# Kernel optimization log

Measured on AMD Instinct MI355X. Metric: run time of the kernel, lower is better.

## Reference

```python
import jax, jax.numpy as jnp
import numpy as np

L, B, T, D, H, A, F, V, BIAS_DIM, E = 6, 16, 512, 512, 8, 64, 2048, 10000, 4, 200000
LN_EPS = 1e-3  # keras LayerNormalization default


def positional_encoding(d, max_len):
    pos = np.arange(max_len, dtype=np.float32)[:, None]
    i = np.arange(d, dtype=np.float32)[None, :]
    angle = pos / np.power(10000.0, (2.0 * np.floor(i / 2.0)) / d)
    pe = np.where((np.arange(d) % 2) == 0, np.sin(angle), np.cos(angle))
    return jnp.asarray(pe, jnp.float32)


def layer_norm(x, g, b):
    mu = jnp.mean(x, -1, keepdims=True)
    var = jnp.mean(jnp.square(x - mu), -1, keepdims=True)
    return (x - mu) * jax.lax.rsqrt(var + LN_EPS) * g + b


def attention(x, masks, bias_idx, Wq, Wk, Wv, Wo, be, bs):
    q = jnp.einsum('btd,dha->btha', x, Wq)
    k = jnp.einsum('btd,dha->btha', x, Wk)
    v = jnp.einsum('btd,dha->btha', x, Wv)
    alpha = jnp.einsum('bkha,bqha->bhqk', k, q)
    # sparse edge bias: scalar per edge = bias_embs[type] @ bias_scalar
    ev = (be[bias_idx[:, 0]] @ bs)[:, 0]                      # [E]
    dense = jnp.zeros((x.shape[0], x.shape[1], x.shape[1]), x.dtype)
    dense = dense.at[bias_idx[:, 1], bias_idx[:, 2], bias_idx[:, 3]].add(ev)  # scatter_nd semantics (add)
    ksum = jnp.sum(k, -1)                                     # [B,T,H]
    alpha = alpha + jnp.einsum('bqk,bkh->bhqk', dense, ksum)
    alpha = alpha * jax.lax.rsqrt(jnp.float32(A))
    alpha = alpha * masks + (1.0 - jnp.ceil(masks)) * jnp.finfo(jnp.float32).min
    alpha = jax.nn.softmax(alpha, -1)
    ctx = jnp.einsum('bhqk,bkha->bqha', alpha, v)
    return jnp.einsum('btha,had->btd', ctx, Wo)


def setup_inputs() -> dict:
    key = jax.random.key(0)
    ks = jax.random.split(key, 24)
    tokens = jax.random.randint(ks[0], (B, T), 0, V, dtype=jnp.int32)
    masks = jnp.ones((B, 1, T, T), jnp.float32)
    ab = jnp.stack([
        jax.random.randint(ks[1], (E,), 0, BIAS_DIM, dtype=jnp.int32),
        jax.random.randint(ks[2], (E,), 0, B, dtype=jnp.int32),
        jax.random.randint(ks[3], (E,), 0, T, dtype=jnp.int32),
        jax.random.randint(ks[4], (E,), 0, T, dtype=jnp.int32)], axis=1)
    s = 0.03
    return {
        'tokens': tokens, 'masks': masks, 'attention_bias': ab,
        'embed': jax.random.normal(ks[5], (V, D)) * (D ** -0.5),
        'Wq': jax.random.normal(ks[6], (L, D, H, A)) * s,
        'Wk': jax.random.normal(ks[7], (L, D, H, A)) * s,
        'Wv': jax.random.normal(ks[8], (L, D, H, A)) * s,
        'Wo': jax.random.normal(ks[9], (L, H, A, D)) * s,
        'be': jax.random.normal(ks[10], (L, BIAS_DIM, A)) * s,
        'bs': jax.random.normal(ks[11], (L, A, 1)) * s,
        'ln_g': jnp.ones((L, 2, D)), 'ln_b': jnp.zeros((L, 2, D)),
        'ff1_w': jax.random.normal(ks[12], (L, D, F)) * s,
        'ff1_b': jnp.zeros((L, F)),
        'ff2_w': jax.random.normal(ks[13], (L, F, D)) * s,
        'ff2_b': jnp.zeros((L, D)),
        'lnout_g': jnp.ones((D,)), 'lnout_b': jnp.zeros((D,)),
    }


def reference(tokens, masks, attention_bias, embed, Wq, Wk, Wv, Wo, be, bs,
              ln_g, ln_b, ff1_w, ff1_b, ff2_w, ff2_b, lnout_g, lnout_b):
    pos_enc = positional_encoding(D, 5000)
    x = embed[tokens] * jnp.sqrt(jnp.float32(D)) + pos_enc[:T]
    for l in range(L):
        h = layer_norm(x, ln_g[l, 0], ln_b[l, 0])
        x = x + attention(h, masks, attention_bias, Wq[l], Wk[l], Wv[l], Wo[l], be[l], bs[l])
        h = layer_norm(x, ln_g[l, 1], ln_b[l, 1])
        x = x + jax.nn.relu(h @ ff1_w[l] + ff1_b[l]) @ ff2_w[l] + ff2_b[l]
    return layer_norm(x, lnout_g, lnout_b)
```

## Files before the change

kernel.cpp:

```cpp
#include <hip/hip_runtime.h>
#include <hip/hip_bf16.h>

#define LNUM 6
#define BB 16
#define TT 512
#define DD 512
#define HH 8
#define AA 64
#define FFD 2048
#define EE 200000
#define BIASDIM 4
#define ATT_NEG (-3.402823466e38f)

typedef __bf16 bf16_t;
typedef __attribute__((ext_vector_type(8))) __bf16 bf16x8;
typedef __attribute__((ext_vector_type(4))) float f32x4;

typedef __attribute__((address_space(3))) void lds_void;
typedef const __attribute__((address_space(1))) void glb_void;

__device__ __forceinline__ void async_load16(const bf16_t* g, bf16_t* l) {
    __builtin_amdgcn_global_load_lds((glb_void*)g, (lds_void*)l, 16, 0, 0);
}

__global__ __launch_bounds__(256) void embed_pe_kernel(
    const int* __restrict__ tokens, const float* __restrict__ embed,
    float* __restrict__ x)
{
    int idx = blockIdx.x * 256 + threadIdx.x;
    int d  = idx & (DD - 1);
    int bt = idx >> 9;
    int t  = bt & (TT - 1);
    int tok = tokens[bt];
    float e = embed[(long long)tok * DD + d] * 22.62741699796952f;
    float p = (float)(2 * (d >> 1)) * (1.0f / (float)DD);
    float denom = exp2f(p * 13.287712379549449f);
    float angle = (float)t / denom;
    float pe = (d & 1) ? cosf(angle) : sinf(angle);
    x[idx] = e + pe;
}

template <typename TO>
__global__ __launch_bounds__(256) void ln_kernel(
    const float* __restrict__ x, TO* __restrict__ y,
    const float* __restrict__ g, const float* __restrict__ b)
{
    long long row = blockIdx.x;
    const float* xr = x + row * DD;
    int tid = threadIdx.x;
    float v0 = xr[tid], v1 = xr[tid + 256];
    float s = v0 + v1, sq = v0 * v0 + v1 * v1;
#pragma unroll
    for (int o = 32; o > 0; o >>= 1) {
        s  += __shfl_down(s, o);
        sq += __shfl_down(sq, o);
    }
    __shared__ float ss[4], sq4[4];
    if ((tid & 63) == 0) { ss[tid >> 6] = s; sq4[tid >> 6] = sq; }
    __syncthreads();
    float st  = ss[0] + ss[1] + ss[2] + ss[3];
    float sqt = sq4[0] + sq4[1] + sq4[2] + sq4[3];
    float mean = st * (1.0f / DD);
    float var  = sqt * (1.0f / DD) - mean * mean;
    float inv  = rsqrtf(var + 1e-3f);
    y[row * DD + tid]       = (TO)((v0 - mean) * inv * g[tid]       + b[tid]);
    y[row * DD + tid + 256] = (TO)((v1 - mean) * inv * g[tid + 256] + b[tid + 256]);
}

template <typename TO, int S>
__global__ __launch_bounds__(256) void reduce_ln_kernel(
    float* __restrict__ x, const float* __restrict__ P,
    TO* __restrict__ y, const float* __restrict__ g, const float* __restrict__ b)
{
    const long long NXc = (long long)BB * TT * DD;
    long long row = blockIdx.x;
    int tid = threadIdx.x;
    long long i0 = row * DD + tid;
    float v0 = x[i0], v1 = x[i0 + 256];
#pragma unroll
    for (int s = 0; s < S; s++) {
        v0 += P[(long long)s * NXc + i0];
        v1 += P[(long long)s * NXc + i0 + 256];
    }
    x[i0] = v0; x[i0 + 256] = v1;
    float s2 = v0 + v1, sq = v0 * v0 + v1 * v1;
#pragma unroll
    for (int o = 32; o > 0; o >>= 1) {
        s2 += __shfl_down(s2, o);
        sq += __shfl_down(sq, o);
    }
    __shared__ float ss[4], sq4[4];
    if ((tid & 63) == 0) { ss[tid >> 6] = s2; sq4[tid >> 6] = sq; }
    __syncthreads();
    float st  = ss[0] + ss[1] + ss[2] + ss[3];
    float sqt = sq4[0] + sq4[1] + sq4[2] + sq4[3];
    float mean = st * (1.0f / DD);
    float var  = sqt * (1.0f / DD) - mean * mean;
    float inv  = rsqrtf(var + 1e-3f);
    y[i0]       = (TO)((v0 - mean) * inv * g[tid]       + b[tid]);
    y[i0 + 256] = (TO)((v1 - mean) * inv * g[tid + 256] + b[tid + 256]);
}

__global__ __launch_bounds__(256) void ksum_kernel(
    const bf16_t* __restrict__ k, float* __restrict__ ks)
{
    int idx = blockIdx.x * 256 + threadIdx.x;
    long long base = (long long)idx * AA;
    float s = 0.f;
#pragma unroll
    for (int a = 0; a < AA; a++) s += (float)k[base + a];
    ks[idx] = s;
}

__global__ __launch_bounds__(256) void bias_scatter_kernel(
    const int* __restrict__ ab, const float* __restrict__ be,
    const float* __restrict__ bs, float* __restrict__ dense)
{
    __shared__ float ev[BIASDIM];
    int tid = threadIdx.x;
    if (tid < BIASDIM) {
        float s = 0.f;
        for (int a = 0; a < AA; a++) s += be[tid * AA + a] * bs[a];
        ev[tid] = s;
    }
    __syncthreads();
    int e = blockIdx.x * 256 + tid;
    if (e < EE) {
        int ty = ab[e * 4 + 0];
        int b  = ab[e * 4 + 1];
        int q  = ab[e * 4 + 2];
        int kk = ab[e * 4 + 3];
        atomicAdd(&dense[((long long)b * TT + q) * TT + kk], ev[ty]);
    }
}

__global__ __launch_bounds__(256) void wconv_kernel(
    const float* __restrict__ in, bf16_t* __restrict__ out, int R, int Cc)
{
    __shared__ bf16_t tile[64][65];
    int c0 = blockIdx.x * 64, r0 = blockIdx.y * 64;
    int tid = threadIdx.x;
#pragma unroll
    for (int i = 0; i < 16; i++) {
        int idx = tid + i * 256; int r = idx >> 6, c = idx & 63;
        tile[c][r] = (bf16_t)in[(long long)(r0 + r) * Cc + c0 + c];
    }
    __syncthreads();
#pragma unroll
    for (int i = 0; i < 16; i++) {
        int idx = tid + i * 256; int rr = idx >> 6, cc = idx & 63;
        out[(long long)(c0 + rr) * R + r0 + cc] = tile[rr][cc];
    }
}

struct Ptr4 { const float* p[4]; };

__global__ __launch_bounds__(256) void wconv4_kernel(Ptr4 srcs, bf16_t* __restrict__ out)
{
    __shared__ bf16_t tile[64][65];
    int z = blockIdx.z;
    const float* in = srcs.p[z];
    bf16_t* o = out + (long long)z * DD * DD;
    int c0 = blockIdx.x * 64, r0 = blockIdx.y * 64;
    int tid = threadIdx.x;
#pragma unroll
    for (int i = 0; i < 16; i++) {
        int idx = tid + i * 256; int r = idx >> 6, c = idx & 63;
        tile[c][r] = (bf16_t)in[(long long)(r0 + r) * DD + c0 + c];
    }
    __syncthreads();
#pragma unroll
    for (int i = 0; i < 16; i++) {
        int idx = tid + i * 256; int rr = idx >> 6, cc = idx & 63;
        o[(long long)(c0 + rr) * DD + r0 + cc] = tile[rr][cc];
    }
}

__global__ __launch_bounds__(256) void vtrans_kernel(
    const bf16_t* __restrict__ v, bf16_t* __restrict__ vT)
{
    __shared__ bf16_t tile[64][65];
    int bh = blockIdx.y; int b = bh >> 3, h = bh & 7;
    int t0 = blockIdx.x * 64;
    int tid = threadIdx.x;
#pragma unroll
    for (int i = 0; i < 16; i++) {
        int idx = tid + i * 256; int r = idx >> 6, c = idx & 63;
        tile[c][r] = v[((long long)(b * TT + t0 + r) * HH + h) * AA + c];
    }
    __syncthreads();
#pragma unroll
    for (int i = 0; i < 16; i++) {
        int idx = tid + i * 256; int a = idx >> 6, t2 = idx & 63;
        vT[(((long long)b * HH + h) * AA + a) * TT + t0 + t2] = tile[a][t2];
    }
}

__global__ __launch_bounds__(256) void fused_attn_kernel(
    const bf16_t* __restrict__ qg, const bf16_t* __restrict__ kg,
    const bf16_t* __restrict__ vT, const float* __restrict__ dense,
    const float* __restrict__ ksum, const float* __restrict__ masks,
    bf16_t* __restrict__ ctx)
{
    __shared__ __align__(16) bf16_t Ks[64 * 64];
    __shared__ __align__(16) bf16_t Vs[64 * 64];
    __shared__ __align__(16) bf16_t Plds[4 * 16 * 88];

    int tid = threadIdx.x;
    int wave = tid >> 6, lane = tid & 63;
    int row16 = lane & 15, quad = lane >> 4;
    int bh = blockIdx.y; int b = bh >> 3, h = bh & 7;
    int qw = blockIdx.x * 64 + wave * 16;

    bf16x8 qf[2];
    {
        const bf16_t* qp = qg + (((long long)b * TT + qw + row16) * HH + h) * AA + quad * 8;
        qf[0] = *(const bf16x8*)(qp);
        qf[1] = *(const bf16x8*)(qp + 32);
    }

    f32x4 o[4] = {};
    float m_r[4], l_r[4];
#pragma unroll
    for (int r = 0; r < 4; r++) { m_r[r] = -3.0e38f; l_r[r] = 0.f; }

    bf16_t* Pw = Plds + wave * 16 * 88;
    const float* dbase = dense + (long long)b * TT * TT;
    const float* mbase = masks + (long long)b * TT * TT;

    for (int kt = 0; kt < 8; kt++) {
        int t0 = kt * 64;
#pragma unroll
        for (int p = tid; p < 512; p += 256) {
            int r = p >> 3, s = p & 7, c = s ^ (r & 7);
            async_load16(kg + (((long long)b * TT + t0 + r) * HH + h) * AA + c * 8,
                         Ks + p * 8);
        }
#pragma unroll
        for (int p = tid; p < 512; p += 256) {
            int r = p >> 3, s = p & 7, c = s ^ (r & 7);
            async_load16(vT + ((long long)bh * AA + r) * TT + t0 + c * 8,
                         Vs + p * 8);
        }
        __syncthreads();

        f32x4 s4[4] = {};
#pragma unroll
        for (int n = 0; n < 4; n++) {
            int row = n * 16 + row16;
            int sw = row & 7;
            bf16x8 kf0 = *(const bf16x8*)(Ks + row * 64 + ((quad ^ sw) * 8));
            bf16x8 kf1 = *(const bf16x8*)(Ks + row * 64 + (((quad + 4) ^ sw) * 8));
            s4[n] = __builtin_amdgcn_mfma_f32_16x16x32_bf16(qf[0], kf0, s4[n], 0, 0, 0);
            s4[n] = __builtin_amdgcn_mfma_f32_16x16x32_bf16(qf[1], kf1, s4[n], 0, 0, 0);
        }

        float val[4][4];
#pragma unroll
        for (int n = 0; n < 4; n++) {
            int ktok = t0 + n * 16 + row16;
            float ksv = ksum[((long long)b * TT + ktok) * HH + h];
#pragma unroll
            for (int r = 0; r < 4; r++) {
                int qgl = qw + quad * 4 + r;
                float d  = dbase[(long long)qgl * TT + ktok];
                float mk = mbase[(long long)qgl * TT + ktok];
                float vv = 0.125f * fmaf(d, ksv, s4[n][r]);
                val[n][r] = vv * mk + (1.0f - ceilf(mk)) * ATT_NEG;
            }
        }

        float scl[4];
#pragma unroll
        for (int r = 0; r < 4; r++) {
            float mx = fmaxf(fmaxf(val[0][r], val[1][r]), fmaxf(val[2][r], val[3][r]));
#pragma unroll
            for (int off = 1; off < 16; off <<= 1) mx = fmaxf(mx, __shfl_xor(mx, off));
            float mnew = fmaxf(m_r[r], mx);
            float sc = __expf(m_r[r] - mnew);
            float ps = 0.f;
#pragma unroll
            for (int n = 0; n < 4; n++) {
                float p = __expf(val[n][r] - mnew);
                val[n][r] = p;
                ps += p;
            }
#pragma unroll
            for (int off = 1; off < 16; off <<= 1) ps += __shfl_xor(ps, off);
            l_r[r] = l_r[r] * sc + ps;
            m_r[r] = mnew;
            scl[r] = sc;
        }
#pragma unroll
        for (int j = 0; j < 4; j++)
#pragma unroll
            for (int r = 0; r < 4; r++) o[j][r] *= scl[r];

#pragma unroll
        for (int n = 0; n < 4; n++)
#pragma unroll
            for (int r = 0; r < 4; r++)
                Pw[(quad * 4 + r) * 88 + n * 16 + row16] = (bf16_t)val[n][r];
        asm volatile("s_waitcnt lgkmcnt(0)" ::: "memory");

        bf16x8 pa0 = *(const bf16x8*)(Pw + row16 * 88 + quad * 8);
        bf16x8 pa1 = *(const bf16x8*)(Pw + row16 * 88 + 32 + quad * 8);
#pragma unroll
        for (int j = 0; j < 4; j++) {
            int row = j * 16 + row16;
            int sw = row & 7;
            bf16x8 vb0 = *(const bf16x8*)(Vs + row * 64 + ((quad ^ sw) * 8));
            bf16x8 vb1 = *(const bf16x8*)(Vs + row * 64 + (((quad + 4) ^ sw) * 8));
            o[j] = __builtin_amdgcn_mfma_f32_16x16x32_bf16(pa0, vb0, o[j], 0, 0, 0);
            o[j] = __builtin_amdgcn_mfma_f32_16x16x32_bf16(pa1, vb1, o[j], 0, 0, 0);
        }
        __syncthreads();
    }

#pragma unroll
    for (int r = 0; r < 4; r++) {
        float invl = 1.0f / l_r[r];
        int qgl = qw + quad * 4 + r;
        bf16_t* cp = ctx + (((long long)b * TT + qgl) * HH + h) * AA;
#pragma unroll
        for (int j = 0; j < 4; j++)
            cp[j * 16 + row16] = (bf16_t)(o[j][r] * invl);
    }
}

template <int BM, int BN, typename TC>
__global__ __launch_bounds__((BM / 64) * (BN / 64) * 64) void gemm_mfma(
    const bf16_t* __restrict__ Ag, const bf16_t* __restrict__ Bg, TC* __restrict__ Cg,
    int K, int lda, int ldb, int ldc,
    long long sAz, long long sBz, long long sCz,
    const float* __restrict__ bias, int accum, int relu)
{
    constexpr int WN = BN / 64;
    constexpr int NT = (BM / 64) * (BN / 64) * 64;
    __shared__ __align__(16) bf16_t As[2][BM * 32];
    __shared__ __align__(16) bf16_t Bs[2][BN * 32];

    int z = blockIdx.z;
    Ag += z * sAz; Bg += z * sBz; Cg += z * sCz;

    int tid = threadIdx.x;
    int wave = tid >> 6, lane = tid & 63;
    int wm = (wave / WN) * 64, wn = (wave % WN) * 64;
    int m0 = blockIdx.x * BM, n0 = blockIdx.y * BN;
    int row16 = lane & 15, quad = lane >> 4;

    f32x4 acc[4][4] = {};

#pragma unroll
    for (int p = tid; p < BM * 4; p += NT) {
        int r = p >> 2, c = p & 3;
        async_load16(Ag + (long long)(m0 + r) * lda + c * 8, As[0] + p * 8);
    }
#pragma unroll
    for (int p = tid; p < BN * 4; p += NT) {
        int r = p >> 2, c = p & 3;
        async_load16(Bg + (long long)(n0 + r) * ldb + c * 8, Bs[0] + p * 8);
    }

    int ib = 0;
    for (int k0 = 0; k0 < K; k0 += 32, ib ^= 1) {
        __syncthreads();
        if (k0 + 32 < K) {
            int kn = k0 + 32;
#pragma unroll
            for (int p = tid; p < BM * 4; p += NT) {
                int r = p >> 2, c = p & 3;
                async_load16(Ag + (long long)(m0 + r) * lda + kn + c * 8,
                             As[ib ^ 1] + p * 8);
            }
#pragma unroll
            for (int p = tid; p < BN * 4; p += NT) {
                int r = p >> 2, c = p & 3;
                async_load16(Bg + (long long)(n0 + r) * ldb + kn + c * 8,
                             Bs[ib ^ 1] + p * 8);
            }
        }
        bf16x8 af[4], bfr[4];
#pragma unroll
        for (int i = 0; i < 4; i++)
            af[i] = *(const bf16x8*)(As[ib] + (wm + i * 16 + row16) * 32 + quad * 8);
#pragma unroll
        for (int j = 0; j < 4; j++)
            bfr[j] = *(const bf16x8*)(Bs[ib] + (wn + j * 16 + row16) * 32 + quad * 8);
#pragma unroll
        for (int i = 0; i < 4; i++)
#pragma unroll
            for (int j = 0; j < 4; j++)
                acc[i][j] = __builtin_amdgcn_mfma_f32_16x16x32_bf16(
                    af[i], bfr[j], acc[i][j], 0, 0, 0);
    }

#pragma unroll
    for (int i = 0; i < 4; i++) {
#pragma unroll
        for (int j = 0; j < 4; j++) {
#pragma unroll
            for (int r = 0; r < 4; r++) {
                int m = m0 + wm + i * 16 + quad * 4 + r;
                int n = n0 + wn + j * 16 + row16;
                float vv = acc[i][j][r];
                if (bias) vv += bias[n];
                if (accum) vv += (float)Cg[(long long)m * ldc + n];
                if (relu) vv = fmaxf(vv, 0.f);
                Cg[(long long)m * ldc + n] = (TC)vv;
            }
        }
    }
}

template <int BM, int BN, int SPLIT>
__global__ __launch_bounds__((BM / 64) * (BN / 64) * 64) void gemm_splitk(
    const bf16_t* __restrict__ Ag, const bf16_t* __restrict__ Bg,
    float* __restrict__ Cg, float* __restrict__ Pg,
    int K, int lda, int ldb, int ldc, const float* __restrict__ bias)
{
    constexpr int WN = BN / 64;
    constexpr int NT = (BM / 64) * (BN / 64) * 64;
    __shared__ __align__(16) bf16_t As[2][BM * 32];
    __shared__ __align__(16) bf16_t Bs[2][BN * 32];

    int z = blockIdx.z;
    int kc = K / SPLIT;
    int kbeg = z * kc, kend = kbeg + kc;

    int tid = threadIdx.x;
    int wave = tid >> 6, lane = tid & 63;
    int wm = (wave / WN) * 64, wn = (wave % WN) * 64;
    int m0 = blockIdx.x * BM, n0 = blockIdx.y * BN;
    int row16 = lane & 15, quad = lane >> 4;

    f32x4 acc[4][4] = {};

#pragma unroll
    for (int p = tid; p < BM * 4; p += NT) {
        int r = p >> 2, c = p & 3;
        async_load16(Ag + (long long)(m0 + r) * lda + kbeg + c * 8, As[0] + p * 8);
    }
#pragma unroll
    for (int p = tid; p < BN * 4; p += NT) {
        int r = p >> 2, c = p & 3;
        async_load16(Bg + (long long)(n0 + r) * ldb + kbeg + c * 8, Bs[0] + p * 8);
    }

    int ib = 0;
    for (int k0 = kbeg; k0 < kend; k0 += 32, ib ^= 1) {
        __syncthreads();
        if (k0 + 32 < kend) {
            int kn = k0 + 32;
#pragma unroll
            for (int p = tid; p < BM * 4; p += NT) {
                int r = p >> 2, c = p & 3;
                async_load16(Ag + (long long)(m0 + r) * lda + kn + c * 8,
                             As[ib ^ 1] + p * 8);
            }
#pragma unroll
            for (int p = tid; p < BN * 4; p += NT) {
                int r = p >> 2, c = p & 3;
                async_load16(Bg + (long long)(n0 + r) * ldb + kn + c * 8,
                             Bs[ib ^ 1] + p * 8);
            }
        }
        bf16x8 af[4], bfr[4];
#pragma unroll
        for (int i = 0; i < 4; i++)
            af[i] = *(const bf16x8*)(As[ib] + (wm + i * 16 + row16) * 32 + quad * 8);
#pragma unroll
        for (int j = 0; j < 4; j++)
            bfr[j] = *(const bf16x8*)(Bs[ib] + (wn + j * 16 + row16) * 32 + quad * 8);
#pragma unroll
        for (int i = 0; i < 4; i++)
#pragma unroll
            for (int j = 0; j < 4; j++)
                acc[i][j] = __builtin_amdgcn_mfma_f32_16x16x32_bf16(
                    af[i], bfr[j], acc[i][j], 0, 0, 0);
    }

    const long long NXc = (long long)BB * TT * DD;
#pragma unroll
    for (int i = 0; i < 4; i++) {
#pragma unroll
        for (int j = 0; j < 4; j++) {
#pragma unroll
            for (int r = 0; r < 4; r++) {
                int m = m0 + wm + i * 16 + quad * 4 + r;
                int n = n0 + wn + j * 16 + row16;
                float vv = acc[i][j][r];
                if (z == 0) {
                    if (bias) vv += bias[n];
                    long long ci = (long long)m * ldc + n;
                    Cg[ci] = Cg[ci] + vv;
                } else {
                    Pg[(long long)(z - 1) * NXc + (long long)m * ldc + n] = vv;
                }
            }
        }
    }
}

extern "C" void kernel_launch(void* const* d_in, const int* in_sizes, int n_in,
                              void* d_out, int out_size, void* d_ws, size_t ws_size,
                              hipStream_t stream)
{
    const int*   tokens = (const int*)d_in[0];
    const float* masks  = (const float*)d_in[1];
    const int*   ab     = (const int*)d_in[2];
    const float* embed  = (const float*)d_in[3];
    const float* Wq     = (const float*)d_in[4];
    const float* Wk     = (const float*)d_in[5];
    const float* Wv     = (const float*)d_in[6];
    const float* Wo     = (const float*)d_in[7];
    const float* be     = (const float*)d_in[8];
    const float* bs     = (const float*)d_in[9];
    const float* ln_g   = (const float*)d_in[10];
    const float* ln_b   = (const float*)d_in[11];
    const float* ff1w   = (const float*)d_in[12];
    const float* ff1b   = (const float*)d_in[13];
    const float* ff2w   = (const float*)d_in[14];
    const float* ff2b   = (const float*)d_in[15];
    const float* lng    = (const float*)d_in[16];
    const float* lnb    = (const float*)d_in[17];
    float* out = (float*)d_out;

    const long long NX = (long long)BB * TT * DD;
    float* x     = (float*)d_ws;
    float* ks    = x + NX;
    bf16_t* h_bf = (bf16_t*)(ks + (long long)BB * TT * HH);
    float* dense = (float*)(h_bf + NX);
    bf16_t* q    = (bf16_t*)(dense + (long long)BB * TT * TT);
    bf16_t* k    = q + NX;
    bf16_t* v    = k + NX;
    bf16_t* vT   = v + NX;
    bf16_t* wqT  = vT + NX;
    bf16_t* wkT  = wqT + (long long)DD * DD;
    bf16_t* wvT  = wkT + (long long)DD * DD;
    bf16_t* woT  = wvT + (long long)DD * DD;
    bf16_t* ff1T = woT + (long long)DD * DD;
    bf16_t* ff2T = ff1T + (long long)DD * FFD;
    bf16_t* ffm  = ff2T + (long long)FFD * DD;

    float* partCtx = dense;
    float* partFF  = dense;

    embed_pe_kernel<<<dim3(NX / 256), dim3(256), 0, stream>>>(tokens, embed, x);

    for (int l = 0; l < LNUM; l++) {
        if (l == 0) {
            ln_kernel<bf16_t><<<dim3(BB * TT), dim3(256), 0, stream>>>(
                x, h_bf, ln_g + (l * 2 + 0) * DD, ln_b + (l * 2 + 0) * DD);
        } else {
            reduce_ln_kernel<bf16_t, 3><<<dim3(BB * TT), dim3(256), 0, stream>>>(
                x, partFF, h_bf, ln_g + (l * 2 + 0) * DD, ln_b + (l * 2 + 0) * DD);
        }

        Ptr4 p4;
        p4.p[0] = Wq + (long long)l * DD * HH * AA;
        p4.p[1] = Wk + (long long)l * DD * HH * AA;
        p4.p[2] = Wv + (long long)l * DD * HH * AA;
        p4.p[3] = Wo + (long long)l * HH * AA * DD;
        wconv4_kernel<<<dim3(8, 8, 4), dim3(256), 0, stream>>>(p4, wqT);
        wconv_kernel<<<dim3(FFD / 64, DD / 64, 1), dim3(256), 0, stream>>>(
            ff1w + (long long)l * DD * FFD, ff1T, DD, FFD);
        wconv_kernel<<<dim3(DD / 64, FFD / 64, 1), dim3(256), 0, stream>>>(
            ff2w + (long long)l * FFD * DD, ff2T, FFD, DD);

        const float* ff1b_l = ff1b + (long long)l * FFD;
        const float* ff2b_l = ff2b + (long long)l * DD;

        gemm_mfma<128, 128, bf16_t><<<dim3(64, 4, 3), dim3(256), 0, stream>>>(
            h_bf, wqT, q, 512, 512, 512, 512,
            0LL, (long long)DD * DD, NX, nullptr, 0, 0);

        vtrans_kernel<<<dim3(8, BB * HH), dim3(256), 0, stream>>>(v, vT);
        ksum_kernel<<<dim3(BB * TT * HH / 256), dim3(256), 0, stream>>>(k, ks);

        hipMemsetAsync(dense, 0, sizeof(float) * (size_t)BB * TT * TT, stream);
        bias_scatter_kernel<<<dim3((EE + 255) / 256), dim3(256), 0, stream>>>(
            ab, be + (long long)l * BIASDIM * AA, bs + (long long)l * AA, dense);

        fused_attn_kernel<<<dim3(TT / 64, BB * HH), dim3(256), 0, stream>>>(
            q, k, vT, dense, ks, masks, h_bf);

        gemm_splitk<128, 64, 2><<<dim3(64, 8, 2), dim3(128), 0, stream>>>(
            h_bf, woT, x, partCtx, 512, 512, 512, 512, nullptr);

        reduce_ln_kernel<bf16_t, 1><<<dim3(BB * TT), dim3(256), 0, stream>>>(
            x, partCtx, h_bf, ln_g + (l * 2 + 1) * DD, ln_b + (l * 2 + 1) * DD);

        gemm_mfma<128, 128, bf16_t><<<dim3(64, 16, 1), dim3(256), 0, stream>>>(
            h_bf, ff1T, ffm, 512, 512, 512, 2048, 0LL, 0LL, 0LL, ff1b_l, 0, 1);

        gemm_splitk<128, 64, 4><<<dim3(64, 8, 4), dim3(128), 0, stream>>>(
            ffm, ff2T, x, partFF, 2048, 2048, 2048, 512, ff2b_l);
    }

    reduce_ln_kernel<float, 3><<<dim3(BB * TT), dim3(256), 0, stream>>>(
        x, partFF, out, lng, lnb);
}
```

Baseline: 1.705 ms.

## Replace split-K partial buffers with atomic accumulation into residual

Split-K GEMMs for the output projection and FF2 now add their partial results straight into the fp32 residual with unsafe float atomics, instead of writing partial slabs that a later reduce+LayerNorm kernel sums. This drops the partial-buffer writes and reads and lets the plain LayerNorm kernel replace the reduce variant. The FF2 GEMM also moves to a 128x128 tile. The bias-scatter atomic likewise switches to unsafeAtomicAdd. The cost is atomic traffic to global memory and a summation order that is no longer deterministic.

```diff
diff --git a/kernel.cpp b/kernel.cpp
--- a/kernel.cpp
+++ b/kernel.cpp
@@ -67,40 +67,6 @@
     y[row * DD + tid + 256] = (TO)((v1 - mean) * inv * g[tid + 256] + b[tid + 256]);
 }
 
-template <typename TO, int S>
-__global__ __launch_bounds__(256) void reduce_ln_kernel(
-    float* __restrict__ x, const float* __restrict__ P,
-    TO* __restrict__ y, const float* __restrict__ g, const float* __restrict__ b)
-{
-    const long long NXc = (long long)BB * TT * DD;
-    long long row = blockIdx.x;
-    int tid = threadIdx.x;
-    long long i0 = row * DD + tid;
-    float v0 = x[i0], v1 = x[i0 + 256];
-#pragma unroll
-    for (int s = 0; s < S; s++) {
-        v0 += P[(long long)s * NXc + i0];
-        v1 += P[(long long)s * NXc + i0 + 256];
-    }
-    x[i0] = v0; x[i0 + 256] = v1;
-    float s2 = v0 + v1, sq = v0 * v0 + v1 * v1;
-#pragma unroll
-    for (int o = 32; o > 0; o >>= 1) {
-        s2 += __shfl_down(s2, o);
-        sq += __shfl_down(sq, o);
-    }
-    __shared__ float ss[4], sq4[4];
-    if ((tid & 63) == 0) { ss[tid >> 6] = s2; sq4[tid >> 6] = sq; }
-    __syncthreads();
-    float st  = ss[0] + ss[1] + ss[2] + ss[3];
-    float sqt = sq4[0] + sq4[1] + sq4[2] + sq4[3];
-    float mean = st * (1.0f / DD);
-    float var  = sqt * (1.0f / DD) - mean * mean;
-    float inv  = rsqrtf(var + 1e-3f);
-    y[i0]       = (TO)((v0 - mean) * inv * g[tid]       + b[tid]);
-    y[i0 + 256] = (TO)((v1 - mean) * inv * g[tid + 256] + b[tid + 256]);
-}
-
 __global__ __launch_bounds__(256) void ksum_kernel(
     const bf16_t* __restrict__ k, float* __restrict__ ks)
 {
@@ -130,7 +96,7 @@
         int b  = ab[e * 4 + 1];
         int q  = ab[e * 4 + 2];
         int kk = ab[e * 4 + 3];
-        atomicAdd(&dense[((long long)b * TT + q) * TT + kk], ev[ty]);
+        unsafeAtomicAdd(&dense[((long long)b * TT + q) * TT + kk], ev[ty]);
     }
 }
 
@@ -414,9 +380,9 @@
 }
 
 template <int BM, int BN, int SPLIT>
-__global__ __launch_bounds__((BM / 64) * (BN / 64) * 64) void gemm_splitk(
+__global__ __launch_bounds__((BM / 64) * (BN / 64) * 64) void gemm_atomic(
     const bf16_t* __restrict__ Ag, const bf16_t* __restrict__ Bg,
-    float* __restrict__ Cg, float* __restrict__ Pg,
+    float* __restrict__ Cg,
     int K, int lda, int ldb, int ldc, const float* __restrict__ bias)
 {
     constexpr int WN = BN / 64;
@@ -480,7 +446,6 @@
                     af[i], bfr[j], acc[i][j], 0, 0, 0);
     }
 
-    const long long NXc = (long long)BB * TT * DD;
 #pragma unroll
     for (int i = 0; i < 4; i++) {
 #pragma unroll
@@ -490,13 +455,8 @@
                 int m = m0 + wm + i * 16 + quad * 4 + r;
                 int n = n0 + wn + j * 16 + row16;
                 float vv = acc[i][j][r];
-                if (z == 0) {
-                    if (bias) vv += bias[n];
-                    long long ci = (long long)m * ldc + n;
-                    Cg[ci] = Cg[ci] + vv;
-                } else {
-                    Pg[(long long)(z - 1) * NXc + (long long)m * ldc + n] = vv;
-                }
+                if (z == 0 && bias) vv += bias[n];
+                unsafeAtomicAdd(&Cg[(long long)m * ldc + n], vv);
             }
         }
     }
@@ -543,19 +503,11 @@
     bf16_t* ff2T = ff1T + (long long)DD * FFD;
     bf16_t* ffm  = ff2T + (long long)FFD * DD;
 
-    float* partCtx = dense;
-    float* partFF  = dense;
-
     embed_pe_kernel<<<dim3(NX / 256), dim3(256), 0, stream>>>(tokens, embed, x);
 
     for (int l = 0; l < LNUM; l++) {
-        if (l == 0) {
-            ln_kernel<bf16_t><<<dim3(BB * TT), dim3(256), 0, stream>>>(
-                x, h_bf, ln_g + (l * 2 + 0) * DD, ln_b + (l * 2 + 0) * DD);
-        } else {
-            reduce_ln_kernel<bf16_t, 3><<<dim3(BB * TT), dim3(256), 0, stream>>>(
-                x, partFF, h_bf, ln_g + (l * 2 + 0) * DD, ln_b + (l * 2 + 0) * DD);
-        }
+        ln_kernel<bf16_t><<<dim3(BB * TT), dim3(256), 0, stream>>>(
+            x, h_bf, ln_g + (l * 2 + 0) * DD, ln_b + (l * 2 + 0) * DD);
 
         Ptr4 p4;
         p4.p[0] = Wq + (long long)l * DD * HH * AA;
@@ -585,19 +537,18 @@
         fused_attn_kernel<<<dim3(TT / 64, BB * HH), dim3(256), 0, stream>>>(
             q, k, vT, dense, ks, masks, h_bf);
 
-        gemm_splitk<128, 64, 2><<<dim3(64, 8, 2), dim3(128), 0, stream>>>(
-            h_bf, woT, x, partCtx, 512, 512, 512, 512, nullptr);
-
-        reduce_ln_kernel<bf16_t, 1><<<dim3(BB * TT), dim3(256), 0, stream>>>(
-            x, partCtx, h_bf, ln_g + (l * 2 + 1) * DD, ln_b + (l * 2 + 1) * DD);
+        gemm_atomic<128, 64, 2><<<dim3(64, 8, 2), dim3(128), 0, stream>>>(
+            h_bf, woT, x, 512, 512, 512, 512, nullptr);
+
+        ln_kernel<bf16_t><<<dim3(BB * TT), dim3(256), 0, stream>>>(
+            x, h_bf, ln_g + (l * 2 + 1) * DD, ln_b + (l * 2 + 1) * DD);
 
         gemm_mfma<128, 128, bf16_t><<<dim3(64, 16, 1), dim3(256), 0, stream>>>(
             h_bf, ff1T, ffm, 512, 512, 512, 2048, 0LL, 0LL, 0LL, ff1b_l, 0, 1);
 
-        gemm_splitk<128, 64, 4><<<dim3(64, 8, 4), dim3(128), 0, stream>>>(
-            ffm, ff2T, x, partFF, 2048, 2048, 2048, 512, ff2b_l);
-    }
-
-    reduce_ln_kernel<float, 3><<<dim3(BB * TT), dim3(256), 0, stream>>>(
-        x, partFF, out, lng, lnb);
-}
+        gemm_atomic<128, 128, 4><<<dim3(64, 4, 4), dim3(256), 0, stream>>>(
+            ffm, ff2T, x, 2048, 2048, 2048, 512, ff2b_l);
+    }
+
+    ln_kernel<float><<<dim3(BB * TT), dim3(256), 0, stream>>>(x, out, lng, lnb);
+}
```

Measured after the change: 1.758 ms. 3.1% more time.

## Replace GEMMs with 256x256-tile, BK=64 swizzled-LDS kernel and drop Wo split-K

Applied to the files above, without the earlier changes.

All projection and FFN GEMMs move to a new 512-thread kernel. It uses 256x256 output tiles, a 64-wide K step, XOR-swizzled LDS staging in 128KB of dynamic shared memory, and a fragment-reuse MFMA ordering, to raise arithmetic intensity per LDS load. The output projection now accumulates straight into x instead of using split-K plus a reduce kernel, so a plain layernorm follows it. The bias scatter switches to unsafeAtomicAdd for cheaper float atomics. The larger tiles cut the block count sharply (64 to 256 blocks per GEMM), which risks leaving many CUs idle.

```diff
diff --git a/kernel.cpp b/kernel.cpp
--- a/kernel.cpp
+++ b/kernel.cpp
@@ -130,7 +130,7 @@
         int b  = ab[e * 4 + 1];
         int q  = ab[e * 4 + 2];
         int kk = ab[e * 4 + 3];
-        atomicAdd(&dense[((long long)b * TT + q) * TT + kk], ev[ty]);
+        unsafeAtomicAdd(&dense[((long long)b * TT + q) * TT + kk], ev[ty]);
     }
 }
 
@@ -328,174 +328,159 @@
     }
 }
 
-template <int BM, int BN, typename TC>
-__global__ __launch_bounds__((BM / 64) * (BN / 64) * 64) void gemm_mfma(
+#define STAGE8(kc0, cb)                                                       \
+    {                                                                         \
+        bf16_t* At = sm + (cb) * 16384;                                       \
+        bf16_t* Bt = sm + 32768 + (cb) * 16384;                               \
+        _Pragma("unroll")                                                     \
+        for (int i = 0; i < 4; i++) {                                         \
+            int qq = tid + i * 512;                                           \
+            int r = (qq >> 3) & 127, hf = qq >> 10, ck = qq & 7;              \
+            int cc = (kc0) + ((ck ^ (r & 7)) * 8);                            \
+            async_load16(Ag + (long long)(m0 + hf * 128 + r) * lda + cc,      \
+                         At + qq * 8);                                        \
+            async_load16(Bg + (long long)(n0 + hf * 128 + r) * ldb + cc,      \
+                         Bt + qq * 8);                                        \
+        }                                                                     \
+    }
+
+#define LOADA8(mh)                                                            \
+    _Pragma("unroll")                                                         \
+    for (int mf = 0; mf < 4; mf++) {                                          \
+        int ra = (mh) * 64 + mf * 16 + row16;                                 \
+        _Pragma("unroll")                                                     \
+        for (int ks2 = 0; ks2 < 2; ks2++)                                     \
+            a8[mf][ks2] = *(const bf16x8*)(Ac + ra * 64 +                     \
+                             (((ks2 * 4 + quad) ^ (ra & 7)) * 8));            \
+    }
+
+#define LOADB8(nh)                                                            \
+    _Pragma("unroll")                                                         \
+    for (int nf = 0; nf < 2; nf++) {                                          \
+        int rb = (wn & 1) * 64 + (nh) * 32 + nf * 16 + row16;                 \
+        _Pragma("unroll")                                                     \
+        for (int ks2 = 0; ks2 < 2; ks2++)                                     \
+            b8[nf][ks2] = *(const bf16x8*)(Bc + rb * 64 +                     \
+                             (((ks2 * 4 + quad) ^ (rb & 7)) * 8));            \
+    }
+
+#define MM8(mh, nh)                                                           \
+    _Pragma("unroll")                                                         \
+    for (int mf = 0; mf < 4; mf++)                                            \
+        _Pragma("unroll")                                                     \
+        for (int nf = 0; nf < 2; nf++)                                        \
+            _Pragma("unroll")                                                 \
+            for (int ks2 = 0; ks2 < 2; ks2++)                                 \
+                acc[(mh) * 4 + mf][(nh) * 2 + nf] =                           \
+                    __builtin_amdgcn_mfma_f32_16x16x32_bf16(                  \
+                        a8[mf][ks2], b8[nf][ks2],                             \
+                        acc[(mh) * 4 + mf][(nh) * 2 + nf], 0, 0, 0);
+
+template <typename TC, int ACCUM, int RELU>
+__global__ __launch_bounds__(512, 2) void gemm8(
     const bf16_t* __restrict__ Ag, const bf16_t* __restrict__ Bg, TC* __restrict__ Cg,
     int K, int lda, int ldb, int ldc,
     long long sAz, long long sBz, long long sCz,
-    const float* __restrict__ bias, int accum, int relu)
-{
-    constexpr int WN = BN / 64;
-    constexpr int NT = (BM / 64) * (BN / 64) * 64;
-    __shared__ __align__(16) bf16_t As[2][BM * 32];
-    __shared__ __align__(16) bf16_t Bs[2][BN * 32];
-
+    const float* __restrict__ bias)
+{
+    extern __shared__ __align__(16) bf16_t sm[];
     int z = blockIdx.z;
     Ag += z * sAz; Bg += z * sBz; Cg += z * sCz;
 
     int tid = threadIdx.x;
     int wave = tid >> 6, lane = tid & 63;
-    int wm = (wave / WN) * 64, wn = (wave % WN) * 64;
-    int m0 = blockIdx.x * BM, n0 = blockIdx.y * BN;
+    int wm = wave >> 2, wn = wave & 3;
     int row16 = lane & 15, quad = lane >> 4;
-
-    f32x4 acc[4][4] = {};
-
-#pragma unroll
-    for (int p = tid; p < BM * 4; p += NT) {
-        int r = p >> 2, c = p & 3;
-        async_load16(Ag + (long long)(m0 + r) * lda + c * 8, As[0] + p * 8);
-    }
-#pragma unroll
-    for (int p = tid; p < BN * 4; p += NT) {
-        int r = p >> 2, c = p & 3;
-        async_load16(Bg + (long long)(n0 + r) * ldb + c * 8, Bs[0] + p * 8);
-    }
-
-    int ib = 0;
-    for (int k0 = 0; k0 < K; k0 += 32, ib ^= 1) {
+    int m0 = blockIdx.x * 256, n0 = blockIdx.y * 256;
+
+    f32x4 acc[8][4] = {};
+
+    int nt = K >> 6;
+    STAGE8(0, 0);
+    __syncthreads();
+
+    int c = 0;
+    for (int t = 0; t < nt; ++t, c ^= 1) {
+        if (t + 1 < nt) STAGE8((t + 1) * 64, c ^ 1);
+        const bf16_t* Ac = sm + c * 16384 + wm * 8192;
+        const bf16_t* Bc = sm + 32768 + c * 16384 + (wn >> 1) * 8192;
+        bf16x8 a8[4][2], b8[2][2];
+        LOADA8(0); LOADB8(0); MM8(0, 0);
+        LOADB8(1);            MM8(0, 1);
+        LOADA8(1);            MM8(1, 1);
+        LOADB8(0);            MM8(1, 0);
         __syncthreads();
-        if (k0 + 32 < K) {
-            int kn = k0 + 32;
-#pragma unroll
-            for (int p = tid; p < BM * 4; p += NT) {
-                int r = p >> 2, c = p & 3;
-                async_load16(Ag + (long long)(m0 + r) * lda + kn + c * 8,
-                             As[ib ^ 1] + p * 8);
-            }
-#pragma unroll
-            for (int p = tid; p < BN * 4; p += NT) {
-                int r = p >> 2, c = p & 3;
-                async_load16(Bg + (long long)(n0 + r) * ldb + kn + c * 8,
-                             Bs[ib ^ 1] + p * 8);
-            }
-        }
-        bf16x8 af[4], bfr[4];
-#pragma unroll
-        for (int i = 0; i < 4; i++)
-            af[i] = *(const bf16x8*)(As[ib] + (wm + i * 16 + row16) * 32 + quad * 8);
-#pragma unroll
-        for (int j = 0; j < 4; j++)
-            bfr[j] = *(const bf16x8*)(Bs[ib] + (wn + j * 16 + row16) * 32 + quad * 8);
-#pragma unroll
-        for (int i = 0; i < 4; i++)
-#pragma unroll
-            for (int j = 0; j < 4; j++)
-                acc[i][j] = __builtin_amdgcn_mfma_f32_16x16x32_bf16(
-                    af[i], bfr[j], acc[i][j], 0, 0, 0);
-    }
-
-#pragma unroll
-    for (int i = 0; i < 4; i++) {
+    }
+
+#pragma unroll
+    for (int i = 0; i < 8; i++) {
 #pragma unroll
         for (int j = 0; j < 4; j++) {
 #pragma unroll
             for (int r = 0; r < 4; r++) {
-                int m = m0 + wm + i * 16 + quad * 4 + r;
-                int n = n0 + wn + j * 16 + row16;
+                int m = m0 + wm * 128 + i * 16 + quad * 4 + r;
+                int n = n0 + wn * 64 + j * 16 + row16;
                 float vv = acc[i][j][r];
                 if (bias) vv += bias[n];
-                if (accum) vv += (float)Cg[(long long)m * ldc + n];
-                if (relu) vv = fmaxf(vv, 0.f);
+                if (ACCUM) vv += (float)Cg[(long long)m * ldc + n];
+                if (RELU) vv = fmaxf(vv, 0.f);
                 Cg[(long long)m * ldc + n] = (TC)vv;
             }
         }
     }
 }
 
-template <int BM, int BN, int SPLIT>
-__global__ __launch_bounds__((BM / 64) * (BN / 64) * 64) void gemm_splitk(
+template <int SPLIT>
+__global__ __launch_bounds__(512, 2) void gemm8_splitk(
     const bf16_t* __restrict__ Ag, const bf16_t* __restrict__ Bg,
     float* __restrict__ Cg, float* __restrict__ Pg,
     int K, int lda, int ldb, int ldc, const float* __restrict__ bias)
 {
-    constexpr int WN = BN / 64;
-    constexpr int NT = (BM / 64) * (BN / 64) * 64;
-    __shared__ __align__(16) bf16_t As[2][BM * 32];
-    __shared__ __align__(16) bf16_t Bs[2][BN * 32];
-
+    extern __shared__ __align__(16) bf16_t sm[];
     int z = blockIdx.z;
-    int kc = K / SPLIT;
-    int kbeg = z * kc, kend = kbeg + kc;
+    int kbeg = z * (K / SPLIT);
 
     int tid = threadIdx.x;
     int wave = tid >> 6, lane = tid & 63;
-    int wm = (wave / WN) * 64, wn = (wave % WN) * 64;
-    int m0 = blockIdx.x * BM, n0 = blockIdx.y * BN;
+    int wm = wave >> 2, wn = wave & 3;
     int row16 = lane & 15, quad = lane >> 4;
-
-    f32x4 acc[4][4] = {};
-
-#pragma unroll
-    for (int p = tid; p < BM * 4; p += NT) {
-        int r = p >> 2, c = p & 3;
-        async_load16(Ag + (long long)(m0 + r) * lda + kbeg + c * 8, As[0] + p * 8);
-    }
-#pragma unroll
-    for (int p = tid; p < BN * 4; p += NT) {
-        int r = p >> 2, c = p & 3;
-        async_load16(Bg + (long long)(n0 + r) * ldb + kbeg + c * 8, Bs[0] + p * 8);
-    }
-
-    int ib = 0;
-    for (int k0 = kbeg; k0 < kend; k0 += 32, ib ^= 1) {
+    int m0 = blockIdx.x * 256, n0 = blockIdx.y * 256;
+
+    f32x4 acc[8][4] = {};
+
+    int nt = (K / SPLIT) >> 6;
+    STAGE8(kbeg, 0);
+    __syncthreads();
+
+    int c = 0;
+    for (int t = 0; t < nt; ++t, c ^= 1) {
+        if (t + 1 < nt) STAGE8(kbeg + (t + 1) * 64, c ^ 1);
+        const bf16_t* Ac = sm + c * 16384 + wm * 8192;
+        const bf16_t* Bc = sm + 32768 + c * 16384 + (wn >> 1) * 8192;
+        bf16x8 a8[4][2], b8[2][2];
+        LOADA8(0); LOADB8(0); MM8(0, 0);
+        LOADB8(1);            MM8(0, 1);
+        LOADA8(1);            MM8(1, 1);
+        LOADB8(0);            MM8(1, 0);
         __syncthreads();
-        if (k0 + 32 < kend) {
-            int kn = k0 + 32;
-#pragma unroll
-            for (int p = tid; p < BM * 4; p += NT) {
-                int r = p >> 2, c = p & 3;
-                async_load16(Ag + (long long)(m0 + r) * lda + kn + c * 8,
-                             As[ib ^ 1] + p * 8);
-            }
-#pragma unroll
-            for (int p = tid; p < BN * 4; p += NT) {
-                int r = p >> 2, c = p & 3;
-                async_load16(Bg + (long long)(n0 + r) * ldb + kn + c * 8,
-                             Bs[ib ^ 1] + p * 8);
-            }
-        }
-        bf16x8 af[4], bfr[4];
-#pragma unroll
-        for (int i = 0; i < 4; i++)
-            af[i] = *(const bf16x8*)(As[ib] + (wm + i * 16 + row16) * 32 + quad * 8);
-#pragma unroll
-        for (int j = 0; j < 4; j++)
-            bfr[j] = *(const bf16x8*)(Bs[ib] + (wn + j * 16 + row16) * 32 + quad * 8);
-#pragma unroll
-        for (int i = 0; i < 4; i++)
-#pragma unroll
-            for (int j = 0; j < 4; j++)
-                acc[i][j] = __builtin_amdgcn_mfma_f32_16x16x32_bf16(
-                    af[i], bfr[j], acc[i][j], 0, 0, 0);
     }
 
     const long long NXc = (long long)BB * TT * DD;
 #pragma unroll
-    for (int i = 0; i < 4; i++) {
+    for (int i = 0; i < 8; i++) {
 #pragma unroll
         for (int j = 0; j < 4; j++) {
 #pragma unroll
             for (int r = 0; r < 4; r++) {
-                int m = m0 + wm + i * 16 + quad * 4 + r;
-                int n = n0 + wn + j * 16 + row16;
+                int m = m0 + wm * 128 + i * 16 + quad * 4 + r;
+                int n = n0 + wn * 64 + j * 16 + row16;
                 float vv = acc[i][j][r];
+                long long ci = (long long)m * ldc + n;
                 if (z == 0) {
                     if (bias) vv += bias[n];
-                    long long ci = (long long)m * ldc + n;
                     Cg[ci] = Cg[ci] + vv;
                 } else {
-                    Pg[(long long)(z - 1) * NXc + (long long)m * ldc + n] = vv;
+                    Pg[(long long)(z - 1) * NXc + ci] = vv;
                 }
             }
         }
@@ -543,8 +528,9 @@
     bf16_t* ff2T = ff1T + (long long)DD * FFD;
     bf16_t* ffm  = ff2T + (long long)FFD * DD;
 
-    float* partCtx = dense;
-    float* partFF  = dense;
+    float* partFF = dense;
+
+    const size_t LDS8 = 131072;
 
     embed_pe_kernel<<<dim3(NX / 256), dim3(256), 0, stream>>>(tokens, embed, x);
 
@@ -571,9 +557,9 @@
         const float* ff1b_l = ff1b + (long long)l * FFD;
         const float* ff2b_l = ff2b + (long long)l * DD;
 
-        gemm_mfma<128, 128, bf16_t><<<dim3(64, 4, 3), dim3(256), 0, stream>>>(
+        gemm8<bf16_t, 0, 0><<<dim3(32, 2, 3), dim3(512), LDS8, stream>>>(
             h_bf, wqT, q, 512, 512, 512, 512,
-            0LL, (long long)DD * DD, NX, nullptr, 0, 0);
+            0LL, (long long)DD * DD, NX, nullptr);
 
         vtrans_kernel<<<dim3(8, BB * HH), dim3(256), 0, stream>>>(v, vT);
         ksum_kernel<<<dim3(BB * TT * HH / 256), dim3(256), 0, stream>>>(k, ks);
@@ -585,16 +571,16 @@
         fused_attn_kernel<<<dim3(TT / 64, BB * HH), dim3(256), 0, stream>>>(
             q, k, vT, dense, ks, masks, h_bf);
 
-        gemm_splitk<128, 64, 2><<<dim3(64, 8, 2), dim3(128), 0, stream>>>(
-            h_bf, woT, x, partCtx, 512, 512, 512, 512, nullptr);
-
-        reduce_ln_kernel<bf16_t, 1><<<dim3(BB * TT), dim3(256), 0, stream>>>(
-            x, partCtx, h_bf, ln_g + (l * 2 + 1) * DD, ln_b + (l * 2 + 1) * DD);
-
-        gemm_mfma<128, 128, bf16_t><<<dim3(64, 16, 1), dim3(256), 0, stream>>>(
-            h_bf, ff1T, ffm, 512, 512, 512, 2048, 0LL, 0LL, 0LL, ff1b_l, 0, 1);
-
-        gemm_splitk<128, 64, 4><<<dim3(64, 8, 4), dim3(128), 0, stream>>>(
+        gemm8<float, 1, 0><<<dim3(32, 2, 1), dim3(512), LDS8, stream>>>(
+            h_bf, woT, x, 512, 512, 512, 512, 0LL, 0LL, 0LL, nullptr);
+
+        ln_kernel<bf16_t><<<dim3(BB * TT), dim3(256), 0, stream>>>(
+            x, h_bf, ln_g + (l * 2 + 1) * DD, ln_b + (l * 2 + 1) * DD);
+
+        gemm8<bf16_t, 0, 1><<<dim3(32, 8, 1), dim3(512), LDS8, stream>>>(
+            h_bf, ff1T, ffm, 512, 512, 512, 2048, 0LL, 0LL, 0LL, ff1b_l);
+
+        gemm8_splitk<4><<<dim3(32, 2, 4), dim3(512), LDS8, stream>>>(
             ffm, ff2T, x, partFF, 2048, 2048, 2048, 512, ff2b_l);
     }
 
```

After: 1.864 ms. +9.3%, slower.
